# Performance work log

Hardware: AMD Instinct MI355X
Metric: run time of the kernel (lower is better)

Reference implementation:

```python
import jax, jax.numpy as jnp
import numpy as np

N = 50000
E = 1600000
# pna_deg histogram: all 50000 nodes have in-degree 32
_DEG_HIST = np.zeros(33, dtype=np.float64); _DEG_HIST[32] = N
AVG_DEG_LOG = float((np.log(np.arange(33) + 1.0) * _DEG_HIST).sum() / _DEG_HIST.sum())


def _segment_softmax(scores, seg, num_segments):
    # PyG softmax: subtract per-segment max, exp, normalize (+1e-16)
    m = jax.ops.segment_max(scores, seg, num_segments)
    e = jnp.exp(scores - m[seg])
    s = jax.ops.segment_sum(e, seg, num_segments)
    return e / (s[seg] + 1e-16)


def _gatv2(x, src, dst, edge_attr, Wl, bl, Wr, br, We, att, bias, H, C, n):
    xl = (x @ Wl + bl).reshape(n, H, C)   # source transform
    xr = (x @ Wr + br).reshape(n, H, C)   # target transform
    ee = (edge_attr @ We).reshape(-1, H, C)
    m = jax.nn.leaky_relu(xl[src] + xr[dst] + ee, negative_slope=0.2)  # [E,H,C]
    alpha = jnp.einsum('ehc,hc->eh', m, att)
    alpha = _segment_softmax(alpha, dst, n)
    out = jax.ops.segment_sum(xl[src] * alpha[:, :, None], dst, n)     # [n,H,C]
    return out.reshape(n, H * C) + bias


def setup_inputs() -> dict:
    key = jax.random.key(0)
    ks = jax.random.split(key, 20)
    x = jax.random.normal(ks[0], (N, 5), jnp.float32)
    src = jax.random.randint(ks[1], (E,), 0, N, jnp.int32)
    dst = ((src + 1 + jax.random.randint(ks[2], (E,), 0, N - 1, jnp.int32)) % N).astype(jnp.int32)
    edge_index = jnp.stack([src, dst])
    edge_weights = jax.random.uniform(ks[3], (E,), jnp.float32)

    def g(k, fi, fo):
        return (jax.random.normal(k, (fi, fo), jnp.float32) / np.sqrt(fi)).astype(jnp.float32)

    return dict(
        x=x, edge_index=edge_index, edge_weights=edge_weights,
        W_ee=g(ks[4], 1, 5), b_ee=jnp.zeros(5, jnp.float32),
        W_pre=g(ks[5], 15, 5), b_pre=jnp.zeros(5, jnp.float32),
        W_post=g(ks[6], 65, 8), b_post=jnp.zeros(8, jnp.float32),
        W_pna=g(ks[7], 8, 8), b_pna=jnp.zeros(8, jnp.float32),
        W1l=g(ks[8], 8, 16), b1l=jnp.zeros(16, jnp.float32),
        W1r=g(ks[9], 8, 16), b1r=jnp.zeros(16, jnp.float32),
        W1e=g(ks[10], 1, 16),
        att1=(jax.random.normal(ks[11], (4, 4), jnp.float32) * 0.5),
        bias1=jnp.zeros(16, jnp.float32),
        W2l=g(ks[12], 16, 32), b2l=jnp.zeros(32, jnp.float32),
        W2r=g(ks[13], 16, 32), b2r=jnp.zeros(32, jnp.float32),
        W2e=g(ks[14], 1, 32),
        att2=(jax.random.normal(ks[15], (4, 8), jnp.float32) / np.sqrt(8.0)).astype(jnp.float32),
        bias2=jnp.zeros(32, jnp.float32),
        Wn=g(ks[16], 32, 32), bn=jnp.zeros(32, jnp.float32),
        We_fc=g(ks[17], 65, 32), be_fc=jnp.zeros(32, jnp.float32),
    )


def reference(x, edge_index, edge_weights,
              W_ee, b_ee, W_pre, b_pre, W_post, b_post, W_pna, b_pna,
              W1l, b1l, W1r, b1r, W1e, att1, bias1,
              W2l, b2l, W2r, b2r, W2e, att2, bias2,
              Wn, bn, We_fc, be_fc):
    n = x.shape[0]
    src, dst = edge_index[0], edge_index[1]
    ea = edge_weights.reshape(-1, 1)  # [E,1]

    # ---------- PNAConv (towers=1, pre/post = single Linear) ----------
    enc = ea @ W_ee + b_ee                               # edge encoder [E,5]
    h = jnp.concatenate([x[dst], x[src], enc], axis=1)   # [x_i, x_j, e] -> [E,15]
    m = h @ W_pre + b_pre                                # [E,5]
    cnt = jax.ops.segment_sum(jnp.ones((m.shape[0],), m.dtype), dst, n)
    cntc = jnp.maximum(cnt, 1.0)[:, None]
    mean = jax.ops.segment_sum(m, dst, n) / cntc
    mean_sq = jax.ops.segment_sum(m * m, dst, n) / cntc
    std = jnp.sqrt(jax.nn.relu(mean_sq - mean * mean) + 1e-5)
    has = (cnt > 0)[:, None]
    mn = jnp.where(has, jax.ops.segment_min(m, dst, n), 0.0)
    mx = jnp.where(has, jax.ops.segment_max(m, dst, n), 0.0)
    agg = jnp.concatenate([mean, mn, mx, std], axis=1)   # [N,20]
    amp = jnp.log(jnp.maximum(cnt, 1.0) + 1.0)[:, None] / AVG_DEG_LOG
    out = jnp.concatenate([x, agg, agg * amp, agg / amp], axis=1)  # [N,65]
    nf = (out @ W_post + b_post) @ W_pna + b_pna         # [N,8]

    # ---------- self loops for GATv2 (fill_value='mean') ----------
    loop = jnp.arange(n, dtype=src.dtype)
    src_sl = jnp.concatenate([src, loop])
    dst_sl = jnp.concatenate([dst, loop])
    ea_mean = jax.ops.segment_sum(ea, dst, n) / cntc     # per-dst mean edge attr
    ea_sl = jnp.concatenate([ea, ea_mean], axis=0)

    nf = jax.nn.relu(_gatv2(nf, src_sl, dst_sl, ea_sl, W1l, b1l, W1r, b1r, W1e, att1, bias1, 4, 4, n))
    nf = jax.nn.relu(_gatv2(nf, src_sl, dst_sl, ea_sl, W2l, b2l, W2r, b2r, W2e, att2, bias2, 4, 8, n))
    nf = jax.nn.relu(nf @ Wn + bn)                       # [N,32]

    ef = jnp.concatenate([ea, nf[src], nf[dst]], axis=1) # [E,65]
    scores = ef @ We_fc + be_fc                          # [E,32]
    s0 = _segment_softmax(scores[:, 0], src, n)          # node_wise_softmax over src
    s1 = _segment_softmax(scores[:, 1], src, n)
    return scores.at[:, 0].set(s0).at[:, 1].set(s1)
```

## Files before the change

kernel.cpp:

```cpp
#include <hip/hip_runtime.h>
#include <math.h>

#define NN 50000
#define NE 1600000
#define AVG_DEG_LOG 3.4965075614664802f
#define NBIN 196
#define CHUNK 4096
#define NCHUNK 391

typedef float f4v __attribute__((ext_vector_type(4)));
typedef _Float16 h4v __attribute__((ext_vector_type(4)));

__device__ __forceinline__ float lrelu(float x){ return x > 0.f ? x : 0.2f*x; }
__device__ __forceinline__ float relu(float x){ return x > 0.f ? x : 0.f; }

__device__ __forceinline__ int ent_node(int2 ent){ return ent.x & 0xFFFF; }
__device__ __forceinline__ int ent_eid(int2 ent){
    return (int)(((unsigned)ent.x >> 16) | ((((unsigned)ent.y >> 19) & 31u) << 16));
}
__device__ __forceinline__ float ent_w(int2 ent){
    return ((float)((unsigned)ent.y & 0x7FFFFu) + 0.5f) * (1.0f/524288.0f);
}
__device__ __forceinline__ unsigned quant_w(float w){
    unsigned wq = (unsigned)(w * 524288.f);
    return wq > 524287u ? 524287u : wq;
}
__device__ __forceinline__ int cent_node(int e){ return e & 0xFFFF; }
__device__ __forceinline__ float cent_w(int e){
    return ((float)(((unsigned)e >> 16) & 0xFFFFu) + 0.5f) * (1.0f/65536.0f);
}
__device__ __forceinline__ unsigned fenc(float f){
    unsigned b = __float_as_uint(f);
    return (b & 0x80000000u) ? ~b : (b | 0x80000000u);
}
__device__ __forceinline__ float fdec(unsigned u){
    unsigned b = (u & 0x80000000u) ? (u & 0x7FFFFFFFu) : ~u;
    return __uint_as_float(b);
}


__global__ __launch_bounds__(256) void k_hist(const int* __restrict__ src, const int* __restrict__ dst,
                                              int* __restrict__ histD, int* __restrict__ histS){
    __shared__ int hd[NBIN], hs[NBIN];
    for (int t=threadIdx.x; t<NBIN; t+=256){ hd[t]=0; hs[t]=0; }
    __syncthreads();
// ... 4 lines not shown
        atomicAdd(&hs[src[e]>>8], 1);
    }
    __syncthreads();
    for (int t=threadIdx.x; t<NBIN; t+=256){
        histD[t*NCHUNK+chunk] = hd[t];
        histS[t*NCHUNK+chunk] = hs[t];
    }
}

__global__ __launch_bounds__(256) void k_binsum(const int* __restrict__ histD, const int* __restrict__ histS,
                                                int* __restrict__ binTotal){
    __shared__ int wsum[4];
    int dir = blockIdx.x / NBIN, bin = blockIdx.x % NBIN;
    const int* hist = dir ? histS : histD;
    int s = 0;
    for (int t=threadIdx.x; t<NCHUNK; t+=256) s += hist[bin*NCHUNK + t];
    #pragma unroll
    for (int st=32; st>=1; st>>=1) s += __shfl_xor(s, st);
    if ((threadIdx.x & 63) == 0) wsum[threadIdx.x>>6] = s;
    __syncthreads();
    if (threadIdx.x == 0) binTotal[dir*NBIN + bin] = wsum[0]+wsum[1]+wsum[2]+wsum[3];
}

__global__ __launch_bounds__(256) void k_scanbins(const int* __restrict__ binTotal,
                                                  int* __restrict__ binStartD, int* __restrict__ binStartS){
    __shared__ int wsums[4];
    int tid = threadIdx.x, lane = tid & 63, wv = tid >> 6;
    for (int dir = 0; dir < 2; ++dir){
        int* binStart = dir ? binStartS : binStartD;
        int v = (tid < NBIN) ? binTotal[dir*NBIN + tid] : 0;
        int sc = v;
        for (int d = 1; d < 64; d <<= 1){
            int t = __shfl_up(sc, d, 64);
            if (lane >= d) sc += t;
        }
        if (lane == 63) wsums[wv] = sc;
        __syncthreads();
        int woff = 0;
        #pragma unroll
        for (int k = 0; k < 4; ++k) woff += (k < wv) ? wsums[k] : 0;
        int excl = woff + sc - v;
        if (tid < NBIN) binStart[tid] = excl;
        if (tid == 0) binStart[NBIN] = NE;
        __syncthreads();
    }
}

__global__ __launch_bounds__(256) void k_chunkpfx(const int* __restrict__ histD, const int* __restrict__ histS,
                                                  const int* __restrict__ binStartD, const int* __restrict__ binStartS,
                                                  int* __restrict__ baseD, int* __restrict__ baseS){
    __shared__ int wsums[4];
    int dir = blockIdx.x / NBIN, bin = blockIdx.x % NBIN;
    const int* hist = dir ? histS : histD;
    const int* binStart = dir ? binStartS : binStartD;
    int* base = dir ? baseS : baseD;
    int tid = threadIdx.x, lane = tid & 63, wv = tid >> 6;
    int i0 = tid*2, i1 = tid*2+1;
    int a = (i0 < NCHUNK) ? hist[bin*NCHUNK + i0] : 0;
    int b = (i1 < NCHUNK) ? hist[bin*NCHUNK + i1] : 0;
    int v = a + b;
    int sc = v;
    for (int d = 1; d < 64; d <<= 1){
        int t = __shfl_up(sc, d, 64);
        if (lane >= d) sc += t;
    }
    if (lane == 63) wsums[wv] = sc;
    __syncthreads();
    int woff = 0;
    #pragma unroll
    for (int k = 0; k < 4; ++k) woff += (k < wv) ? wsums[k] : 0;
    int excl = binStart[bin] + woff + sc - v;
    if (i0 < NCHUNK) base[bin*NCHUNK + i0] = excl;
    if (i1 < NCHUNK) base[bin*NCHUNK + i1] = excl + a;
}

__global__ __launch_bounds__(256) void k_coarse(const int* __restrict__ src, const int* __restrict__ dst,
                                                const float* __restrict__ ea,
                                                const int* __restrict__ baseD, const int* __restrict__ baseS,
                                                int2* __restrict__ cD, int2* __restrict__ cS){
    __shared__ int curd[NBIN], curs[NBIN];
    int chunk = blockIdx.x;
    for (int t=threadIdx.x; t<NBIN; t+=256){
        curd[t] = baseD[t*NCHUNK+chunk];
        curs[t] = baseS[t*NCHUNK+chunk];
    }
    __syncthreads();
    int e0 = chunk*CHUNK, e1 = min(e0+CHUNK, NE);
    for (int e=e0+threadIdx.x; e<e1; e+=256){
        int s = src[e], d = dst[e];
        unsigned wq = quant_w(ea[e]);
        unsigned elo = (unsigned)(e & 0xFFFF) << 16;
        unsigned ehi = ((unsigned)e >> 16) << 19;
        int pd = atomicAdd(&curd[d>>8], 1);
        cD[pd] = make_int2((int)((unsigned)s | elo), (int)(((unsigned)(d & 255) << 24) | ehi | wq));
        int ps = atomicAdd(&curs[s>>8], 1);
        cS[ps] = make_int2((int)((unsigned)d | elo), (int)(((unsigned)(s & 255) << 24) | ehi | wq));
    }
}

__global__ __launch_bounds__(256) void k_fine_d(const int2* __restrict__ cin,
                                                const int* __restrict__ binStart,
                                                int2* __restrict__ bout,
                                                int* __restrict__ cnt, int* __restrict__ off){
    __shared__ int h[256], cur[256];
    __shared__ int ws4[4];
    int bin = blockIdx.x;
    int S = binStart[bin], E = binStart[bin+1];
    h[threadIdx.x] = 0;
    __syncthreads();
    for (int i = S + threadIdx.x; i < E; i += 256){
        unsigned y = (unsigned)cin[i].y;
        atomicAdd(&h[y >> 24], 1);
    }
    __syncthreads();
    int v = h[threadIdx.x];
    int lane = threadIdx.x & 63, wv = threadIdx.x >> 6;
    int sc = v;
    for (int d = 1; d < 64; d <<= 1){
        int t = __shfl_up(sc, d, 64);
        if (lane >= d) sc += t;
    }
    if (lane == 63) ws4[wv] = sc;
    __syncthreads();
    int woff = 0;
    #pragma unroll
    for (int k = 0; k < 4; ++k) woff += (k < wv) ? ws4[k] : 0;
    int excl = woff + sc - v;
    cur[threadIdx.x] = S + excl;
    int node = (bin << 8) + threadIdx.x;
    if (node < NN){ cnt[node] = v; off[node] = S + excl; }
    __syncthreads();
    for (int i = S + threadIdx.x; i < E; i += 256){
        int2 ent = cin[i];
        unsigned y = (unsigned)ent.y;
        int local = y >> 24;
        int pos = atomicAdd(&cur[local], 1);
        bout[pos] = make_int2(ent.x, (int)(y & 0x00FFFFFFu));
    }
}


__global__ void k_zero(int* cnt_d, int* cnt_s){
    int i = blockIdx.x*blockDim.x + threadIdx.x;
    if (i < NN){ cnt_d[i]=0; cnt_s[i]=0; }
}

__global__ void k_count(const int* __restrict__ src, const int* __restrict__ dst,
                        int* cnt_d, int* cnt_s){
    int e = blockIdx.x*blockDim.x + threadIdx.x;
    if (e >= NE) return;
    atomicAdd(&cnt_d[dst[e]], 1);
    atomicAdd(&cnt_s[src[e]], 1);
}

__global__ __launch_bounds__(1024) void k_scanCSR(const int* __restrict__ cnt_d, const int* __restrict__ cnt_s,
                                                  int* off_d, int* cur_d, int* off_s, int* cur_s){
    __shared__ int wsums[16];
    __shared__ int carry_s;
    const int tid = threadIdx.x, lane = tid & 63, wv = tid >> 6;
    const int pass = blockIdx.x;
// ... 15 lines not shown
            if (lane >= d) sc += t;
        }
        if (lane == 63) wsums[wv] = sc;
        __syncthreads();
        int woff = 0;
        #pragma unroll
        for (int k = 0; k < 16; ++k) woff += (k < wv) ? wsums[k] : 0;
        int carry_in = carry_s;
        __syncthreads();
        if (tid == 1023) carry_s = carry_in + woff + sc;
        int excl = carry_in + woff + (sc - tsum);
        int e0 = excl, e1 = e0+v0, e2 = e1+v1, e3 = e2+v2;
        if (i0+0 < NN){ off[i0+0]=e0; cur[i0+0]=e0; }
        if (i0+1 < NN){ off[i0+1]=e1; cur[i0+1]=e1; }
        if (i0+2 < NN){ off[i0+2]=e2; cur[i0+2]=e2; }
        if (i0+3 < NN){ off[i0+3]=e3; cur[i0+3]=e3; }
        __syncthreads();
    }
}

__global__ void k_scatter(const int* __restrict__ src, const int* __restrict__ dst,
                          const float* __restrict__ ea,
                          int* cur_d, int* cur_s,
                          int2* bktd, int* bkts){
    int e = blockIdx.x*blockDim.x + threadIdx.x;
    if (e >= NE) return;
    int s = src[e], d = dst[e];
    unsigned wq = quant_w(ea[e]);
    unsigned elo = (unsigned)(e & 0xFFFF) << 16;
    unsigned yv  = (((unsigned)e >> 16) << 19) | wq;
    int p = atomicAdd(&cur_d[d], 1);
    bktd[p] = make_int2((int)((unsigned)s | elo), (int)yv);
    int q = atomicAdd(&cur_s[s], 1);
    bkts[q] = (int)(((unsigned)d & 0xFFFFu) | ((wq >> 3) << 16));
}

__global__ __launch_bounds__(256) void k_pna(
    const float* __restrict__ x,
    const int* __restrict__ cnt_d, const int* __restrict__ off_d,
    const int2* __restrict__ bktd,
    const float* __restrict__ W_ee, const float* __restrict__ b_ee,
    const float* __restrict__ W_pre, const float* __restrict__ b_pre,
    const float* __restrict__ W_post, const float* __restrict__ b_post,
    const float* __restrict__ W_pna, const float* __restrict__ b_pna,
    const float* __restrict__ W1l, const float* __restrict__ b1l,
    const float* __restrict__ W1r, const float* __restrict__ b1r,
    float* __restrict__ xl1, float* __restrict__ xr1, float* __restrict__ ea_mean)
{
    __shared__ float sWpre[75], sWpost[520], sWpna[64], sW1l[128], sW1r[128];
    __shared__ float sbpre[5], sWee[5], sbee[5], sbpost[8], sbpna[8], sb1l[16], sb1r[16];
    for (int t=threadIdx.x; t<75;  t+=256) sWpre[t]=W_pre[t];
    for (int t=threadIdx.x; t<520; t+=256) sWpost[t]=W_post[t];
    for (int t=threadIdx.x; t<64;  t+=256) sWpna[t]=W_pna[t];
    for (int t=threadIdx.x; t<128; t+=256){ sW1l[t]=W1l[t]; sW1r[t]=W1r[t]; }
    if (threadIdx.x<5){ sbpre[threadIdx.x]=b_pre[threadIdx.x]; sWee[threadIdx.x]=W_ee[threadIdx.x]; sbee[threadIdx.x]=b_ee[threadIdx.x]; }
    if (threadIdx.x<8){ sbpost[threadIdx.x]=b_post[threadIdx.x]; sbpna[threadIdx.x]=b_pna[threadIdx.x]; }
    if (threadIdx.x<16){ sb1l[threadIdx.x]=b1l[threadIdx.x]; sb1r[threadIdx.x]=b1r[threadIdx.x]; }
    __syncthreads();
    int node = blockIdx.x*32 + (threadIdx.x>>3);
    if (node >= NN) return;
    int g = threadIdx.x & 7;
    float xd[5];
    #pragma unroll
    for (int k=0;k<5;k++) xd[k] = x[node*5+k];
    float cb[5], c1v[5];
    #pragma unroll
    for (int c=0;c<5;c++){
        float a = sbpre[c], b = 0.f;
        #pragma unroll
        for (int k=0;k<5;k++){
            a += xd[k]*sWpre[k*5+c];
            a += sbee[k]*sWpre[(10+k)*5+c];
            b += sWee[k]*sWpre[(10+k)*5+c];
        }
        cb[c]=a; c1v[c]=b;
    }
    int deg = cnt_d[node], base = off_d[node];
    float sum[5], ssq[5], mn[5], mx[5];
    #pragma unroll
    for (int c=0;c<5;c++){ sum[c]=0.f; ssq[c]=0.f; mn[c]=1e30f; mx[c]=-1e30f; }
    float wsum = 0.f;
    for (int j=g; j<deg; j+=8){
        int2 ent = bktd[base+j];
        int s = ent_node(ent);
        float w = ent_w(ent);
        wsum += w;
        float xs[5];
        #pragma unroll
        for (int k=0;k<5;k++) xs[k] = x[s*5+k];
        #pragma unroll
        for (int c=0;c<5;c++){
            float m = cb[c] + w*c1v[c];
            #pragma unroll
            for (int k=0;k<5;k++) m += xs[k]*sWpre[(5+k)*5+c];
            sum[c]+=m; ssq[c]+=m*m; mn[c]=fminf(mn[c],m); mx[c]=fmaxf(mx[c],m);
        }
    }
    #pragma unroll
    for (int st=1; st<8; st<<=1){
        #pragma unroll
        for (int c=0;c<5;c++){
            sum[c] += __shfl_xor(sum[c], st);
            ssq[c] += __shfl_xor(ssq[c], st);
            mn[c] = fminf(mn[c], __shfl_xor(mn[c], st));
            mx[c] = fmaxf(mx[c], __shfl_xor(mx[c], st));
        }
        wsum += __shfl_xor(wsum, st);
    }
// ... 15 lines not shown
    for (int j=0;j<20;j++){ feat[25+j]=feat[5+j]*amp; feat[45+j]=feat[5+j]/amp; }
    float t = sbpost[g];
    #pragma unroll
    for (int k=0;k<65;k++) t += feat[k]*sWpost[k*8+g];
    float nf = sbpna[g];
    #pragma unroll
    for (int k=0;k<8;k++) nf += __shfl(t, k, 8) * sWpna[k*8+g];
    float nfk[8];
    #pragma unroll
    for (int k=0;k<8;k++) nfk[k] = __shfl(nf, k, 8);
    #pragma unroll
    for (int u=0;u<2;u++){
        int o = 2*g+u;
        float a=sb1l[o], b2=sb1r[o];
        #pragma unroll
        for (int k=0;k<8;k++){ a += nfk[k]*sW1l[k*16+o]; b2 += nfk[k]*sW1r[k*16+o]; }
        xl1[node*16+o]=a; xr1[node*16+o]=b2;
    }
    if (g==0) ea_mean[node] = wsum/cc;
}

__global__ __launch_bounds__(256) void k_gat1(
    const int* __restrict__ cnt_d, const int* __restrict__ off_d,
    const int2* __restrict__ bktd,
    const float* __restrict__ xl1, const float* __restrict__ xr1,
    const float* __restrict__ ea_mean,
    const float* __restrict__ We1, const float* __restrict__ att1, const float* __restrict__ bias1,
    const float* __restrict__ W2l, const float* __restrict__ b2l,
    const float* __restrict__ W2r, const float* __restrict__ b2r,
    _Float16* __restrict__ xl2h, float* __restrict__ xr2)
{
    __shared__ float sWe[16], sAtt[16], sBias[16], sW2l[512], sW2r[512], sb2l[32], sb2r[32];
    for (int t=threadIdx.x; t<512; t+=256){ sW2l[t]=W2l[t]; sW2r[t]=W2r[t]; }
    if (threadIdx.x<16){ sWe[threadIdx.x]=We1[threadIdx.x]; sAtt[threadIdx.x]=att1[threadIdx.x]; sBias[threadIdx.x]=bias1[threadIdx.x]; }
    if (threadIdx.x<32){ sb2l[threadIdx.x]=b2l[threadIdx.x]; sb2r[threadIdx.x]=b2r[threadIdx.x]; }
    __syncthreads();
    int node = blockIdx.x*32 + (threadIdx.x>>3);
    if (node >= NN) return;
    int g = threadIdx.x & 7;
    float xr[16];
    #pragma unroll
    for (int k=0;k<4;k++){
        float4 v = *(const float4*)(xr1 + node*16 + k*4);
        xr[k*4]=v.x; xr[k*4+1]=v.y; xr[k*4+2]=v.z; xr[k*4+3]=v.w;
    }
    int deg = cnt_d[node], base = off_d[node];
    float eam = ea_mean[node];
    float m[4], ss[4], acc[16];
    #pragma unroll
    for (int h=0;h<4;h++){ m[h]=-1e30f; ss[h]=0.f; }
    #pragma unroll
    for (int k=0;k<16;k++) acc[k]=0.f;
    for (int j=g; j<=deg; j+=8){
        bool selfe = (j==deg);
        int s; float w;
        if (selfe){ s = node; w = eam; }
        else { int2 ent = bktd[base+j]; s = ent_node(ent); w = ent_w(ent); }
        float xls[16];
        #pragma unroll
        for (int k=0;k<4;k++){
            float4 v = *(const float4*)(xl1 + s*16 + k*4);
            xls[k*4]=v.x; xls[k*4+1]=v.y; xls[k*4+2]=v.z; xls[k*4+3]=v.w;
        }
        #pragma unroll
        for (int h=0;h<4;h++){
            float a = 0.f;
            #pragma unroll
            for (int ch=0;ch<4;ch++){
                int idx = h*4+ch;
                a += lrelu(xls[idx] + xr[idx] + w*sWe[idx]) * sAtt[idx];
            }
            float mn2 = fmaxf(m[h], a);
            float corr = __expf(m[h]-mn2);
            float p = __expf(a-mn2);
            ss[h] = ss[h]*corr + p;
            #pragma unroll
            for (int ch=0;ch<4;ch++){
                int idx = h*4+ch;
                acc[idx] = acc[idx]*corr + p*xls[idx];
            }
// ... 21 lines not shown
    float nf1[16];
    #pragma unroll
    for (int h=0;h<4;h++){
        float den = ss[h] + 1e-16f;
        #pragma unroll
        for (int ch=0;ch<4;ch++){
            int idx=h*4+ch;
            nf1[idx] = relu(acc[idx]/den + sBias[idx]);
        }
    }
    #pragma unroll
    for (int u=0;u<4;u++){
        int o = g + 8*u;
        float a=sb2l[o], b=sb2r[o];
        #pragma unroll
        for (int k=0;k<16;k++){ a += nf1[k]*sW2l[k*32+o]; b += nf1[k]*sW2r[k*32+o]; }
        xl2h[(size_t)node*32+o] = (_Float16)a;
        xr2[node*32+o]=b;
    }
}

__global__ __launch_bounds__(256) void k_gat2(
    const int* __restrict__ cnt_d, const int* __restrict__ off_d,
    const int2* __restrict__ bktd,
    const _Float16* __restrict__ xl2h, const float* __restrict__ xr2,
    const float* __restrict__ ea_mean,
    const float* __restrict__ We2, const float* __restrict__ att2, const float* __restrict__ bias2,
    const float* __restrict__ Wn, const float* __restrict__ bn,
    const float* __restrict__ We_fc,
    _Float16* __restrict__ Ps16, float* __restrict__ Pd,
    float* __restrict__ Ps01, float* __restrict__ Pd01)
{
    __shared__ float sWe[32], sAtt[32], sBias[32], sWn[1024], sbn[32];
    __shared__ float sWsrc[1024], sWdst[1024];
    for (int t=threadIdx.x; t<1024; t+=256){
        sWn[t]=Wn[t];
        sWsrc[t]=We_fc[32 + t];
        sWdst[t]=We_fc[33*32 + t];
    }
    if (threadIdx.x<32){ sWe[threadIdx.x]=We2[threadIdx.x]; sAtt[threadIdx.x]=att2[threadIdx.x];
                         sBias[threadIdx.x]=bias2[threadIdx.x]; sbn[threadIdx.x]=bn[threadIdx.x]; }
    __syncthreads();
    int node = blockIdx.x*32 + (threadIdx.x>>3);
    if (node >= NN) return;
    int g = threadIdx.x & 7;
    float xr[32];
    #pragma unroll
    for (int k=0;k<8;k++){
        float4 v = *(const float4*)(xr2 + node*32 + k*4);
        xr[k*4]=v.x; xr[k*4+1]=v.y; xr[k*4+2]=v.z; xr[k*4+3]=v.w;
    }
    int deg = cnt_d[node], base = off_d[node];
    float eam = ea_mean[node];
    float m[4], ss[4], acc[32];
    #pragma unroll
    for (int h=0;h<4;h++){ m[h]=-1e30f; ss[h]=0.f; }
    #pragma unroll
    for (int k=0;k<32;k++) acc[k]=0.f;
    for (int j=g; j<=deg; j+=8){
        bool selfe = (j==deg);
        int s; float w;
        if (selfe){ s = node; w = eam; }
        else { int2 ent = bktd[base+j]; s = ent_node(ent); w = ent_w(ent); }
        float xls[32];
        const h4v* xp = (const h4v*)(xl2h + (size_t)s*32);
        #pragma unroll
        for (int k=0;k<8;k++){
            h4v hv = xp[k];
            xls[k*4]   = (float)hv.x;
            xls[k*4+1] = (float)hv.y;
            xls[k*4+2] = (float)hv.z;
            xls[k*4+3] = (float)hv.w;
        }
        #pragma unroll
        for (int h=0;h<4;h++){
            float a = 0.f;
            #pragma unroll
            for (int ch=0;ch<8;ch++){
                int idx = h*8+ch;
                a += lrelu(xls[idx] + xr[idx] + w*sWe[idx]) * sAtt[idx];
            }
            float mn2 = fmaxf(m[h], a);
            float corr = __expf(m[h]-mn2);
            float p = __expf(a-mn2);
            ss[h] = ss[h]*corr + p;
            #pragma unroll
            for (int ch=0;ch<8;ch++){
                int idx = h*8+ch;
                acc[idx] = acc[idx]*corr + p*xls[idx];
            }
            m[h] = mn2;
        }
    }
    #pragma unroll
    for (int st=1; st<8; st<<=1){
// ... 24 lines not shown
        }
    }
    float mine[4];
    #pragma unroll
    for (int u=0;u<4;u++){
        int oo = g + 8*u;
        float a = sbn[oo];
        #pragma unroll
        for (int k=0;k<32;k++) a += nf2[k]*sWn[k*32+oo];
        mine[u] = relu(a);
    }
    float nfn[32];
    #pragma unroll
    for (int k=0;k<32;k++) nfn[k] = __shfl(mine[k>>3], k&7, 8);
    float pa[4], pb[4];
    #pragma unroll
    for (int u=0;u<4;u++){
        int oo = g + 8*u;
        float a=0.f, b=0.f;
        #pragma unroll
        for (int k=0;k<32;k++){ a += nfn[k]*sWsrc[k*32+oo]; b += nfn[k]*sWdst[k*32+oo]; }
        pa[u]=a; pb[u]=b;
        Ps16[(size_t)node*32+oo] = (_Float16)a;
        Pd[node*32+oo]=b;
    }
    float ps0=__shfl(pa[0],0,8), ps1=__shfl(pa[0],1,8);
    float pd0=__shfl(pb[0],0,8), pd1=__shfl(pb[0],1,8);
    if (g==0){
        *(float2*)(Ps01 + node*2) = make_float2(ps0, ps1);
        *(float2*)(Pd01 + node*2) = make_float2(pd0, pd1);
    }
}

__global__ __launch_bounds__(1024) void k_src_bins(
    const int2* __restrict__ cS, const int* __restrict__ binStartS,
    const float* __restrict__ Ps01, const float* __restrict__ Pd01,
    const float* __restrict__ We_fc, const float* __restrict__ be_fc,
    float* __restrict__ smax, float* __restrict__ sden)
{
    __shared__ float sPs0[256], sPs1[256];
    __shared__ unsigned sM0[256], sM1[256];
    __shared__ float sS0[256], sS1[256];
    __shared__ float cW00, cW01, cbe0, cbe1;
    int bin = blockIdx.x, tid = threadIdx.x;
    if (tid == 0){ cW00=We_fc[0]; cW01=We_fc[1]; cbe0=be_fc[0]; cbe1=be_fc[1]; }
    if (tid < 256){
        int node = (bin<<8) + tid;
        float2 p = (node < NN) ? *(const float2*)(Ps01 + node*2) : make_float2(0.f,0.f);
        sPs0[tid]=p.x; sPs1[tid]=p.y;
        sM0[tid]=fenc(-1e30f); sM1[tid]=fenc(-1e30f);
        sS0[tid]=0.f; sS1[tid]=0.f;
    }
    __syncthreads();
    int S = binStartS[bin], E = binStartS[bin+1];
    for (int i = S + tid; i < E; i += 1024){
        int2 ent = cS[i];
        unsigned y = (unsigned)ent.y;
        int local = y >> 24;
        int d = ent.x & 0xFFFF;
        float w = ((float)(y & 0x7FFFFu) + 0.5f) * (1.0f/524288.0f);
        float2 q = *(const float2*)(Pd01 + d*2);
        float a0 = cbe0 + sPs0[local] + w*cW00 + q.x;
        float a1 = cbe1 + sPs1[local] + w*cW01 + q.y;
        atomicMax(&sM0[local], fenc(a0));
        atomicMax(&sM1[local], fenc(a1));
    }
    __syncthreads();
    for (int i = S + tid; i < E; i += 1024){
        int2 ent = cS[i];
        unsigned y = (unsigned)ent.y;
        int local = y >> 24;
        int d = ent.x & 0xFFFF;
        float w = ((float)(y & 0x7FFFFu) + 0.5f) * (1.0f/524288.0f);
        float2 q = *(const float2*)(Pd01 + d*2);
        float a0 = cbe0 + sPs0[local] + w*cW00 + q.x;
        float a1 = cbe1 + sPs1[local] + w*cW01 + q.y;
        atomicAdd(&sS0[local], __expf(a0 - fdec(sM0[local])));
        atomicAdd(&sS1[local], __expf(a1 - fdec(sM1[local])));
    }
    __syncthreads();
    if (tid < 256){
        int node = (bin<<8) + tid;
        if (node < NN){
            smax[node*2]   = fdec(sM0[tid]);
            smax[node*2+1] = fdec(sM1[tid]);
            sden[node*2]   = sS0[tid];
            sden[node*2+1] = sS1[tid];
        }
    }
}

__global__ __launch_bounds__(256) void k_src(
    const int* __restrict__ cnt_s, const int* __restrict__ off_s,
    const int* __restrict__ bkts,
    const float* __restrict__ Ps01, const float* __restrict__ Pd01,
    const float* __restrict__ We_fc, const float* __restrict__ be_fc,
    float* __restrict__ smax, float* __restrict__ sden)
{
    __shared__ float sW00, sW01, sbe0, sbe1;
    if (threadIdx.x == 0){ sW00=We_fc[0]; sW01=We_fc[1]; sbe0=be_fc[0]; sbe1=be_fc[1]; }
    __syncthreads();
    int node = blockIdx.x*32 + (threadIdx.x>>3);
    if (node >= NN) return;
    int g = threadIdx.x & 7;
    float2 p = *(const float2*)(Ps01 + node*2);
    float base0 = sbe0 + p.x, base1 = sbe1 + p.y;
    int deg = cnt_s[node], base = off_s[node];
    float m0=-1e30f, m1=-1e30f, s0=0.f, s1=0.f;
    for (int j=g; j<deg; j+=8){
        int ent = bkts[base+j];
        int d = cent_node(ent);
        float w = cent_w(ent);
        float2 q = *(const float2*)(Pd01 + d*2);
        float a0 = base0 + w*sW00 + q.x;
        float a1 = base1 + w*sW01 + q.y;
        float mn0 = fmaxf(m0, a0);
        s0 = s0*__expf(m0-mn0) + __expf(a0-mn0); m0 = mn0;
        float mn1 = fmaxf(m1, a1);
        s1 = s1*__expf(m1-mn1) + __expf(a1-mn1); m1 = mn1;
    }
    #pragma unroll
    for (int st=1; st<8; st<<=1){
        float mo = __shfl_xor(m0, st), so = __shfl_xor(s0, st);
        float mn = fmaxf(m0, mo);
        s0 = s0*__expf(m0-mn) + so*__expf(mo-mn); m0 = mn;
        mo = __shfl_xor(m1, st); so = __shfl_xor(s1, st);
        mn = fmaxf(m1, mo);
        s1 = s1*__expf(m1-mn) + so*__expf(mo-mn); m1 = mn;
    }
    if (g==0){ smax[node*2]=m0; smax[node*2+1]=m1; sden[node*2]=s0; sden[node*2+1]=s1; }
}

__global__ __launch_bounds__(256) void k_scC2(
    const int* __restrict__ cnt_d, const int* __restrict__ off_d,
    const int2* __restrict__ bktd,
    const _Float16* __restrict__ Ps16, const float* __restrict__ Pd,
    const float* __restrict__ We_fc, const float* __restrict__ be_fc,
    const float* __restrict__ smax, const float* __restrict__ sden,
    float* __restrict__ out)
{
    __shared__ float sW0[32], sB[32];
    if (threadIdx.x < 32){ sW0[threadIdx.x]=We_fc[threadIdx.x]; sB[threadIdx.x]=be_fc[threadIdx.x]; }
    __syncthreads();
    int node = blockIdx.x*32 + (threadIdx.x>>3);
    if (node >= NN) return;
    int g = threadIdx.x & 7;
    float4 pd = *(const float4*)(Pd + (size_t)node*32 + g*4);
    float4 w0 = *(const float4*)(sW0 + g*4);
    float4 b0 = *(const float4*)(sB + g*4);
    b0.x += pd.x; b0.y += pd.y; b0.z += pd.z; b0.w += pd.w;
    int deg = cnt_d[node], base = off_d[node];
    for (int j=0; j<deg; ++j){
        int2 ent = bktd[base+j];
        int s = ent_node(ent);
        int e = ent_eid(ent);
        float w = ent_w(ent);
        h4v hv = *(const h4v*)(Ps16 + (size_t)s*32 + g*4);
        float ox = b0.x + w*w0.x + (float)hv.x;
        float oy = b0.y + w*w0.y + (float)hv.y;
        float oz = b0.z + w*w0.z + (float)hv.z;
        float ow = b0.w + w*w0.w + (float)hv.w;
        if (g == 0){
            float2 sm = *(const float2*)(smax + s*2);
            float2 sd = *(const float2*)(sden + s*2);
            ox = __expf(ox - sm.x) / (sd.x + 1e-16f);
            oy = __expf(oy - sm.y) / (sd.y + 1e-16f);
        }
        f4v ov; ov.x = ox; ov.y = oy; ov.z = oz; ov.w = ow;
        __builtin_nontemporal_store(ov, (f4v*)(out + (size_t)e*32 + g*4));
    }
}

extern "C" void kernel_launch(void* const* d_in, const int* in_sizes, int n_in,
                              void* d_out, int out_size, void* d_ws, size_t ws_size,
                              hipStream_t stream) {
    const float* x     = (const float*)d_in[0];
    const int*   ei    = (const int*)  d_in[1];
    const float* ea    = (const float*)d_in[2];
    const float* W_ee  = (const float*)d_in[3];  const float* b_ee  = (const float*)d_in[4];
    const float* W_pre = (const float*)d_in[5];  const float* b_pre = (const float*)d_in[6];
    const float* W_post= (const float*)d_in[7];  const float* b_post= (const float*)d_in[8];
    const float* W_pna = (const float*)d_in[9];  const float* b_pna = (const float*)d_in[10];
    const float* W1l   = (const float*)d_in[11]; const float* b1l   = (const float*)d_in[12];
    const float* W1r   = (const float*)d_in[13]; const float* b1r   = (const float*)d_in[14];
    const float* W1e   = (const float*)d_in[15]; const float* att1  = (const float*)d_in[16];
    const float* bias1 = (const float*)d_in[17];
    const float* W2l   = (const float*)d_in[18]; const float* b2l   = (const float*)d_in[19];
    const float* W2r   = (const float*)d_in[20]; const float* b2r   = (const float*)d_in[21];
    const float* W2e   = (const float*)d_in[22]; const float* att2  = (const float*)d_in[23];
    const float* bias2 = (const float*)d_in[24];
    const float* Wn    = (const float*)d_in[25]; const float* bn    = (const float*)d_in[26];
    const float* We_fc = (const float*)d_in[27]; const float* be_fc = (const float*)d_in[28];
    const int* src = ei;
    const int* dst = ei + NE;
    float* out = (float*)d_out;

    float* ws = (float*)d_ws;
    size_t o = 0;
    auto A = [&](size_t n){ size_t r = o; o = (o + n + 63) & ~(size_t)63; return r; };
    int*   cnt_d  = (int*)(ws + A(NN));
    int*   off_d  = (int*)(ws + A(NN));
    int*   cnt_s  = (int*)(ws + A(NN));
    int*   off_s  = (int*)(ws + A(NN));
    int*   cur_d  = (int*)(ws + A(NN));
    int*   cur_s  = (int*)(ws + A(NN));
    float* xl1    =        ws + A((size_t)NN*16);
    float* xr1    =        ws + A((size_t)NN*16);
    _Float16* xl2h = (_Float16*)(ws + A((size_t)NN*16));
    float* xr2    =        ws + A((size_t)NN*32);
    _Float16* Ps16 = (_Float16*)(ws + A((size_t)NN*16));
    float* Pd     =        ws + A((size_t)NN*32);
    float* ea_mean=        ws + A(NN);
    float* Ps01   =        ws + A((size_t)NN*2);
    float* Pd01   =        ws + A((size_t)NN*2);
    float* smax   =        ws + A((size_t)NN*2);
    float* sden   =        ws + A((size_t)NN*2);
    int*   histD  = (int*)(ws + A((size_t)NBIN*NCHUNK));
    int*   histS  = (int*)(ws + A((size_t)NBIN*NCHUNK));
    int*   baseD  = (int*)(ws + A((size_t)NBIN*NCHUNK));
    int*   baseS  = (int*)(ws + A((size_t)NBIN*NCHUNK));
    int*   binTotal  = (int*)(ws + A(2*NBIN));
    int*   binStartD = (int*)(ws + A(NBIN+1));
    int*   binStartS = (int*)(ws + A(NBIN+1));
    int2*  bufX = (int2*)(ws + A(2*(size_t)NE));
    int*   bktsC = (int*)(ws + A((size_t)NE));
    size_t o_fallback = o;
    int2*  bufY = (int2*)(ws + A(2*(size_t)NE));
    int2*  bufZ = (int2*)(ws + A(2*(size_t)NE));
    size_t o_sort = o;
    bool sortmode = (ws_size >= o_sort * sizeof(float));
    if (!sortmode && ws_size < o_fallback * sizeof(float)) return;

    const int BS = 256;
    const int gridE = (NE + BS - 1)/BS;
    const int gridN = (NN + BS - 1)/BS;
    const int gridO = (NN + 31)/32;

    int2* bktd = bufX;
    if (sortmode){
        k_hist<<<NCHUNK, BS, 0, stream>>>(src, dst, histD, histS);
        k_binsum<<<2*NBIN, BS, 0, stream>>>(histD, histS, binTotal);
        k_scanbins<<<1, BS, 0, stream>>>(binTotal, binStartD, binStartS);
        k_chunkpfx<<<2*NBIN, BS, 0, stream>>>(histD, histS, binStartD, binStartS, baseD, baseS);
        k_coarse<<<NCHUNK, BS, 0, stream>>>(src, dst, ea, baseD, baseS, bufY, bufZ);
        k_fine_d<<<NBIN, BS, 0, stream>>>(bufY, binStartD, bufX, cnt_d, off_d);
    } else {
        k_zero<<<gridN, BS, 0, stream>>>(cnt_d, cnt_s);
        k_count<<<gridE, BS, 0, stream>>>(src, dst, cnt_d, cnt_s);
        k_scanCSR<<<2, 1024, 0, stream>>>(cnt_d, cnt_s, off_d, cur_d, off_s, cur_s);
        k_scatter<<<gridE, BS, 0, stream>>>(src, dst, ea, cur_d, cur_s, bufX, bktsC);
    }
    k_pna<<<gridO, BS, 0, stream>>>(x, cnt_d, off_d, bktd,
                                    W_ee, b_ee, W_pre, b_pre, W_post, b_post, W_pna, b_pna,
                                    W1l, b1l, W1r, b1r, xl1, xr1, ea_mean);
    k_gat1<<<gridO, BS, 0, stream>>>(cnt_d, off_d, bktd, xl1, xr1, ea_mean,
                                     W1e, att1, bias1, W2l, b2l, W2r, b2r, xl2h, xr2);
    k_gat2<<<gridO, BS, 0, stream>>>(cnt_d, off_d, bktd, xl2h, xr2, ea_mean,
                                     W2e, att2, bias2, Wn, bn, We_fc,
                                     Ps16, Pd, Ps01, Pd01);
    if (sortmode){
        k_src_bins<<<NBIN, 1024, 0, stream>>>(bufZ, binStartS, Ps01, Pd01, We_fc, be_fc, smax, sden);
    } else {
        k_src<<<gridO, BS, 0, stream>>>(cnt_s, off_s, bktsC, Ps01, Pd01, We_fc, be_fc, smax, sden);
    }
    k_scC2<<<gridO, BS, 0, stream>>>(cnt_d, off_d, bktd, Ps16, Pd, We_fc, be_fc, smax, sden, out);
}
```

Measured before the change: 298.8 us.

## Compact adjacency, fuse bin scan, and compute edge scores in original edge order

The final edge-score kernel now runs one thread per edge in original order, reading src/dst/ea directly instead of walking the dst-sorted adjacency, so output writes become coalesced and edge ids no longer need to be packed. This lets the dst adjacency shrink from int2 to a single int with 16-bit quantized weight, and Pd is stored as fp16. The separate bin scan kernel is folded into the chunk-prefix kernel, softmax stats are packed into one float4, and k_src_bins caches the first few computed scores in registers to avoid recomputing them. The cost is lower-precision Pd and edge weight in the fine path, and gathers of Ps16/Pd16 by random src/dst.

```diff
diff --git a/kernel.cpp b/kernel.cpp
--- a/kernel.cpp
+++ b/kernel.cpp
@@ -9,18 +9,11 @@
 #define NCHUNK 391
 
 typedef float f4v __attribute__((ext_vector_type(4)));
-typedef _Float16 h4v __attribute__((ext_vector_type(4)));
+typedef _Float16 h8v __attribute__((ext_vector_type(8)));
 
 __device__ __forceinline__ float lrelu(float x){ return x > 0.f ? x : 0.2f*x; }
 __device__ __forceinline__ float relu(float x){ return x > 0.f ? x : 0.f; }
 
-__device__ __forceinline__ int ent_node(int2 ent){ return ent.x & 0xFFFF; }
-__device__ __forceinline__ int ent_eid(int2 ent){
-    return (int)(((unsigned)ent.x >> 16) | ((((unsigned)ent.y >> 19) & 31u) << 16));
-}
-__device__ __forceinline__ float ent_w(int2 ent){
-    return ((float)((unsigned)ent.y & 0x7FFFFu) + 0.5f) * (1.0f/524288.0f);
-}
 __device__ __forceinline__ unsigned quant_w(float w){
     unsigned wq = (unsigned)(w * 524288.f);
     return wq > 524287u ? 524287u : wq;
@@ -71,39 +64,33 @@
     if (threadIdx.x == 0) binTotal[dir*NBIN + bin] = wsum[0]+wsum[1]+wsum[2]+wsum[3];
 }
 
-__global__ __launch_bounds__(256) void k_scanbins(const int* __restrict__ binTotal,
-                                                  int* __restrict__ binStartD, int* __restrict__ binStartS){
-    __shared__ int wsums[4];
-    int tid = threadIdx.x, lane = tid & 63, wv = tid >> 6;
-    for (int dir = 0; dir < 2; ++dir){
-        int* binStart = dir ? binStartS : binStartD;
-        int v = (tid < NBIN) ? binTotal[dir*NBIN + tid] : 0;
-        int sc = v;
-        for (int d = 1; d < 64; d <<= 1){
-            int t = __shfl_up(sc, d, 64);
-            if (lane >= d) sc += t;
-        }
-        if (lane == 63) wsums[wv] = sc;
-        __syncthreads();
-        int woff = 0;
-        #pragma unroll
-        for (int k = 0; k < 4; ++k) woff += (k < wv) ? wsums[k] : 0;
-        int excl = woff + sc - v;
-        if (tid < NBIN) binStart[tid] = excl;
-        if (tid == 0) binStart[NBIN] = NE;
-        __syncthreads();
-    }
-}
-
 __global__ __launch_bounds__(256) void k_chunkpfx(const int* __restrict__ histD, const int* __restrict__ histS,
-                                                  const int* __restrict__ binStartD, const int* __restrict__ binStartS,
+                                                  const int* __restrict__ binTotal,
+                                                  int* __restrict__ binStartD, int* __restrict__ binStartS,
                                                   int* __restrict__ baseD, int* __restrict__ baseS){
     __shared__ int wsums[4];
+    __shared__ int sbase;
     int dir = blockIdx.x / NBIN, bin = blockIdx.x % NBIN;
     const int* hist = dir ? histS : histD;
-    const int* binStart = dir ? binStartS : binStartD;
+    int* binStart = dir ? binStartS : binStartD;
     int* base = dir ? baseS : baseD;
     int tid = threadIdx.x, lane = tid & 63, wv = tid >> 6;
+    {
+        int s = 0;
+        for (int k = tid; k < bin; k += 256) s += binTotal[dir*NBIN + k];
+        #pragma unroll
+        for (int st=32; st>=1; st>>=1) s += __shfl_xor(s, st);
+        if (lane == 0) wsums[wv] = s;
+        __syncthreads();
+        if (tid == 0){
+            sbase = wsums[0]+wsums[1]+wsums[2]+wsums[3];
+            binStart[bin] = sbase;
+            if (bin == 0) binStart[NBIN] = NE;
+        }
+        __syncthreads();
+    }
+    int bS = sbase;
+    __syncthreads();
     int i0 = tid*2, i1 = tid*2+1;
     int a = (i0 < NCHUNK) ? hist[bin*NCHUNK + i0] : 0;
     int b = (i1 < NCHUNK) ? hist[bin*NCHUNK + i1] : 0;
@@ -118,7 +105,7 @@
     int woff = 0;
     #pragma unroll
     for (int k = 0; k < 4; ++k) woff += (k < wv) ? wsums[k] : 0;
-    int excl = binStart[bin] + woff + sc - v;
+    int excl = bS + woff + sc - v;
     if (i0 < NCHUNK) base[bin*NCHUNK + i0] = excl;
     if (i1 < NCHUNK) base[bin*NCHUNK + i1] = excl + a;
 }
@@ -138,19 +125,17 @@
     for (int e=e0+threadIdx.x; e<e1; e+=256){
         int s = src[e], d = dst[e];
         unsigned wq = quant_w(ea[e]);
-        unsigned elo = (unsigned)(e & 0xFFFF) << 16;
-        unsigned ehi = ((unsigned)e >> 16) << 19;
         int pd = atomicAdd(&curd[d>>8], 1);
-        cD[pd] = make_int2((int)((unsigned)s | elo), (int)(((unsigned)(d & 255) << 24) | ehi | wq));
+        cD[pd] = make_int2(s, (int)(((unsigned)(d & 255) << 24) | wq));
         int ps = atomicAdd(&curs[s>>8], 1);
-        cS[ps] = make_int2((int)((unsigned)d | elo), (int)(((unsigned)(s & 255) << 24) | ehi | wq));
-    }
-}
-
-__global__ __launch_bounds__(256) void k_fine_d(const int2* __restrict__ cin,
-                                                const int* __restrict__ binStart,
-                                                int2* __restrict__ bout,
-                                                int* __restrict__ cnt, int* __restrict__ off){
+        cS[ps] = make_int2(d, (int)(((unsigned)(s & 255) << 24) | wq));
+    }
+}
+
+__global__ __launch_bounds__(256) void k_fine(const int2* __restrict__ cin,
+                                              const int* __restrict__ binStart,
+                                              int* __restrict__ bout,
+                                              int* __restrict__ cnt, int* __restrict__ off){
     __shared__ int h[256], cur[256];
     __shared__ int ws4[4];
     int bin = blockIdx.x;
@@ -184,7 +169,8 @@
         unsigned y = (unsigned)ent.y;
         int local = y >> 24;
         int pos = atomicAdd(&cur[local], 1);
-        bout[pos] = make_int2(ent.x, (int)(y & 0x00FFFFFFu));
+        unsigned wq16 = (y & 0x7FFFFu) >> 3;
+        bout[pos] = (int)(((unsigned)ent.x & 0xFFFFu) | (wq16 << 16));
     }
 }
 
@@ -246,23 +232,21 @@
 __global__ void k_scatter(const int* __restrict__ src, const int* __restrict__ dst,
                           const float* __restrict__ ea,
                           int* cur_d, int* cur_s,
-                          int2* bktd, int* bkts){
+                          int* bktd, int* bkts){
     int e = blockIdx.x*blockDim.x + threadIdx.x;
     if (e >= NE) return;
     int s = src[e], d = dst[e];
-    unsigned wq = quant_w(ea[e]);
-    unsigned elo = (unsigned)(e & 0xFFFF) << 16;
-    unsigned yv  = (((unsigned)e >> 16) << 19) | wq;
+    unsigned wq16 = quant_w(ea[e]) >> 3;
     int p = atomicAdd(&cur_d[d], 1);
-    bktd[p] = make_int2((int)((unsigned)s | elo), (int)yv);
+    bktd[p] = (int)(((unsigned)s & 0xFFFFu) | (wq16 << 16));
     int q = atomicAdd(&cur_s[s], 1);
-    bkts[q] = (int)(((unsigned)d & 0xFFFFu) | ((wq >> 3) << 16));
+    bkts[q] = (int)(((unsigned)d & 0xFFFFu) | (wq16 << 16));
 }
 
 __global__ __launch_bounds__(256) void k_pna(
     const float* __restrict__ x,
     const int* __restrict__ cnt_d, const int* __restrict__ off_d,
-    const int2* __restrict__ bktd,
+    const int* __restrict__ adjC,
     const float* __restrict__ W_ee, const float* __restrict__ b_ee,
     const float* __restrict__ W_pre, const float* __restrict__ b_pre,
     const float* __restrict__ W_post, const float* __restrict__ b_post,
@@ -305,9 +289,9 @@
     for (int c=0;c<5;c++){ sum[c]=0.f; ssq[c]=0.f; mn[c]=1e30f; mx[c]=-1e30f; }
     float wsum = 0.f;
     for (int j=g; j<deg; j+=8){
-        int2 ent = bktd[base+j];
-        int s = ent_node(ent);
-        float w = ent_w(ent);
+        int ent = adjC[base+j];
+        int s = cent_node(ent);
+        float w = cent_w(ent);
         wsum += w;
         float xs[5];
         #pragma unroll
@@ -369,7 +353,7 @@
 
 __global__ __launch_bounds__(256) void k_gat1(
     const int* __restrict__ cnt_d, const int* __restrict__ off_d,
-    const int2* __restrict__ bktd,
+    const int* __restrict__ adjC,
     const float* __restrict__ xl1, const float* __restrict__ xr1,
     const float* __restrict__ ea_mean,
     const float* __restrict__ We1, const float* __restrict__ att1, const float* __restrict__ bias1,
@@ -402,7 +386,7 @@
         bool selfe = (j==deg);
         int s; float w;
         if (selfe){ s = node; w = eam; }
-        else { int2 ent = bktd[base+j]; s = ent_node(ent); w = ent_w(ent); }
+        else { int ent = adjC[base+j]; s = cent_node(ent); w = cent_w(ent); }
         float xls[16];
         #pragma unroll
         for (int k=0;k<4;k++){
@@ -470,13 +454,13 @@
 
 __global__ __launch_bounds__(256) void k_gat2(
     const int* __restrict__ cnt_d, const int* __restrict__ off_d,
-    const int2* __restrict__ bktd,
+    const int* __restrict__ adjC,
     const _Float16* __restrict__ xl2h, const float* __restrict__ xr2,
     const float* __restrict__ ea_mean,
     const float* __restrict__ We2, const float* __restrict__ att2, const float* __restrict__ bias2,
     const float* __restrict__ Wn, const float* __restrict__ bn,
     const float* __restrict__ We_fc,
-    _Float16* __restrict__ Ps16, float* __restrict__ Pd,
+    _Float16* __restrict__ Ps16, _Float16* __restrict__ Pd16,
     float* __restrict__ Ps01, float* __restrict__ Pd01)
 {
     __shared__ float sWe[32], sAtt[32], sBias[32], sWn[1024], sbn[32];
@@ -509,16 +493,14 @@
         bool selfe = (j==deg);
         int s; float w;
         if (selfe){ s = node; w = eam; }
-        else { int2 ent = bktd[base+j]; s = ent_node(ent); w = ent_w(ent); }
+        else { int ent = adjC[base+j]; s = cent_node(ent); w = cent_w(ent); }
         float xls[32];
-        const h4v* xp = (const h4v*)(xl2h + (size_t)s*32);
-        #pragma unroll
-        for (int k=0;k<8;k++){
-            h4v hv = xp[k];
-            xls[k*4]   = (float)hv.x;
-            xls[k*4+1] = (float)hv.y;
-            xls[k*4+2] = (float)hv.z;
-            xls[k*4+3] = (float)hv.w;
+        const h8v* xp = (const h8v*)(xl2h + (size_t)s*32);
+        #pragma unroll
+        for (int k=0;k<4;k++){
+            h8v hv = xp[k];
+            #pragma unroll
+            for (int u=0;u<8;u++) xls[k*8+u] = (float)hv[u];
         }
         #pragma unroll
         for (int h=0;h<4;h++){
@@ -589,7 +571,7 @@
         for (int k=0;k<32;k++){ a += nfn[k]*sWsrc[k*32+oo]; b += nfn[k]*sWdst[k*32+oo]; }
         pa[u]=a; pb[u]=b;
         Ps16[(size_t)node*32+oo] = (_Float16)a;
-        Pd[node*32+oo]=b;
+        Pd16[(size_t)node*32+oo] = (_Float16)b;
     }
     float ps0=__shfl(pa[0],0,8), ps1=__shfl(pa[0],1,8);
     float pd0=__shfl(pb[0],0,8), pd1=__shfl(pb[0],1,8);
@@ -603,7 +585,7 @@
     const int2* __restrict__ cS, const int* __restrict__ binStartS,
     const float* __restrict__ Ps01, const float* __restrict__ Pd01,
     const float* __restrict__ We_fc, const float* __restrict__ be_fc,
-    float* __restrict__ smax, float* __restrict__ sden)
+    float4* __restrict__ ssd)
 {
     __shared__ float sPs0[256], sPs1[256];
     __shared__ unsigned sM0[256], sM1[256];
@@ -620,40 +602,61 @@
     }
     __syncthreads();
     int S = binStartS[bin], E = binStartS[bin+1];
-    for (int i = S + tid; i < E; i += 1024){
+    const int REG = 9;
+    float ra0[REG], ra1[REG]; int rl[REG];
+    int n = 0;
+    {
+        int idx = S + tid;
+        #pragma unroll
+        for (int it = 0; it < REG; ++it){
+            if (idx < E){
+                int2 ent = cS[idx];
+                unsigned y = (unsigned)ent.y;
+                int local = y >> 24;
+                int d = ent.x;
+                float w = ((float)(y & 0x7FFFFu) + 0.5f) * (1.0f/524288.0f);
+                float2 q = *(const float2*)(Pd01 + d*2);
+                float a0 = cbe0 + sPs0[local] + w*cW00 + q.x;
+                float a1 = cbe1 + sPs1[local] + w*cW01 + q.y;
+                ra0[it]=a0; ra1[it]=a1; rl[it]=local; n = it+1;
+                atomicMax(&sM0[local], fenc(a0));
+                atomicMax(&sM1[local], fenc(a1));
+            }
+            idx += 1024;
+        }
+        for (int i = S + tid + REG*1024; i < E; i += 1024){
+            int2 ent = cS[i];
+            unsigned y = (unsigned)ent.y;
+            int local = y >> 24;
+            int d = ent.x;
+            float w = ((float)(y & 0x7FFFFu) + 0.5f) * (1.0f/524288.0f);
+            float2 q = *(const float2*)(Pd01 + d*2);
+            atomicMax(&sM0[local], fenc(cbe0 + sPs0[local] + w*cW00 + q.x));
+            atomicMax(&sM1[local], fenc(cbe1 + sPs1[local] + w*cW01 + q.y));
+        }
+    }
+    __syncthreads();
+    #pragma unroll
+    for (int it = 0; it < REG; ++it){
+        if (it < n){
+            atomicAdd(&sS0[rl[it]], __expf(ra0[it] - fdec(sM0[rl[it]])));
+            atomicAdd(&sS1[rl[it]], __expf(ra1[it] - fdec(sM1[rl[it]])));
+        }
+    }
+    for (int i = S + tid + REG*1024; i < E; i += 1024){
         int2 ent = cS[i];
         unsigned y = (unsigned)ent.y;
         int local = y >> 24;
-        int d = ent.x & 0xFFFF;
+        int d = ent.x;
         float w = ((float)(y & 0x7FFFFu) + 0.5f) * (1.0f/524288.0f);
         float2 q = *(const float2*)(Pd01 + d*2);
-        float a0 = cbe0 + sPs0[local] + w*cW00 + q.x;
-        float a1 = cbe1 + sPs1[local] + w*cW01 + q.y;
-        atomicMax(&sM0[local], fenc(a0));
-        atomicMax(&sM1[local], fenc(a1));
-    }
-    __syncthreads();
-    for (int i = S + tid; i < E; i += 1024){
-        int2 ent = cS[i];
-        unsigned y = (unsigned)ent.y;
-        int local = y >> 24;
-        int d = ent.x & 0xFFFF;
-        float w = ((float)(y & 0x7FFFFu) + 0.5f) * (1.0f/524288.0f);
-        float2 q = *(const float2*)(Pd01 + d*2);
-        float a0 = cbe0 + sPs0[local] + w*cW00 + q.x;
-        float a1 = cbe1 + sPs1[local] + w*cW01 + q.y;
-        atomicAdd(&sS0[local], __expf(a0 - fdec(sM0[local])));
-        atomicAdd(&sS1[local], __expf(a1 - fdec(sM1[local])));
+        atomicAdd(&sS0[local], __expf(cbe0 + sPs0[local] + w*cW00 + q.x - fdec(sM0[local])));
+        atomicAdd(&sS1[local], __expf(cbe1 + sPs1[local] + w*cW01 + q.y - fdec(sM1[local])));
     }
     __syncthreads();
     if (tid < 256){
         int node = (bin<<8) + tid;
-        if (node < NN){
-            smax[node*2]   = fdec(sM0[tid]);
-            smax[node*2+1] = fdec(sM1[tid]);
-            sden[node*2]   = sS0[tid];
-            sden[node*2+1] = sS1[tid];
-        }
+        if (node < NN) ssd[node] = make_float4(fdec(sM0[tid]), fdec(sM1[tid]), sS0[tid], sS1[tid]);
     }
 }
 
@@ -662,7 +665,7 @@
     const int* __restrict__ bkts,
     const float* __restrict__ Ps01, const float* __restrict__ Pd01,
     const float* __restrict__ We_fc, const float* __restrict__ be_fc,
-    float* __restrict__ smax, float* __restrict__ sden)
+    float4* __restrict__ ssd)
 {
     __shared__ float sW00, sW01, sbe0, sbe1;
     if (threadIdx.x == 0){ sW00=We_fc[0]; sW01=We_fc[1]; sbe0=be_fc[0]; sbe1=be_fc[1]; }
@@ -695,46 +698,43 @@
         mn = fmaxf(m1, mo);
         s1 = s1*__expf(m1-mn) + so*__expf(mo-mn); m1 = mn;
     }
-    if (g==0){ smax[node*2]=m0; smax[node*2+1]=m1; sden[node*2]=s0; sden[node*2+1]=s1; }
-}
-
-__global__ __launch_bounds__(256) void k_scC2(
-    const int* __restrict__ cnt_d, const int* __restrict__ off_d,
-    const int2* __restrict__ bktd,
-    const _Float16* __restrict__ Ps16, const float* __restrict__ Pd,
+    if (g==0) ssd[node] = make_float4(m0, m1, s0, s1);
+}
+
+__global__ __launch_bounds__(256) void k_scF(
+    const int* __restrict__ src, const int* __restrict__ dst, const float* __restrict__ ea,
+    const _Float16* __restrict__ Ps16, const _Float16* __restrict__ Pd16,
     const float* __restrict__ We_fc, const float* __restrict__ be_fc,
-    const float* __restrict__ smax, const float* __restrict__ sden,
+    const float4* __restrict__ ssd,
     float* __restrict__ out)
 {
     __shared__ float sW0[32], sB[32];
     if (threadIdx.x < 32){ sW0[threadIdx.x]=We_fc[threadIdx.x]; sB[threadIdx.x]=be_fc[threadIdx.x]; }
     __syncthreads();
-    int node = blockIdx.x*32 + (threadIdx.x>>3);
-    if (node >= NN) return;
-    int g = threadIdx.x & 7;
-    float4 pd = *(const float4*)(Pd + (size_t)node*32 + g*4);
-    float4 w0 = *(const float4*)(sW0 + g*4);
-    float4 b0 = *(const float4*)(sB + g*4);
-    b0.x += pd.x; b0.y += pd.y; b0.z += pd.z; b0.w += pd.w;
-    int deg = cnt_d[node], base = off_d[node];
-    for (int j=0; j<deg; ++j){
-        int2 ent = bktd[base+j];
-        int s = ent_node(ent);
-        int e = ent_eid(ent);
-        float w = ent_w(ent);
-        h4v hv = *(const h4v*)(Ps16 + (size_t)s*32 + g*4);
-        float ox = b0.x + w*w0.x + (float)hv.x;
-        float oy = b0.y + w*w0.y + (float)hv.y;
-        float oz = b0.z + w*w0.z + (float)hv.z;
-        float ow = b0.w + w*w0.w + (float)hv.w;
-        if (g == 0){
-            float2 sm = *(const float2*)(smax + s*2);
-            float2 sd = *(const float2*)(sden + s*2);
-            ox = __expf(ox - sm.x) / (sd.x + 1e-16f);
-            oy = __expf(oy - sm.y) / (sd.y + 1e-16f);
-        }
-        f4v ov; ov.x = ox; ov.y = oy; ov.z = oz; ov.w = ow;
-        __builtin_nontemporal_store(ov, (f4v*)(out + (size_t)e*32 + g*4));
+    int e = blockIdx.x*blockDim.x + threadIdx.x;
+    if (e >= NE) return;
+    int s = src[e], d = dst[e];
+    float w = ea[e];
+    const h8v* ps = (const h8v*)(Ps16 + (size_t)s*32);
+    const h8v* pd = (const h8v*)(Pd16 + (size_t)d*32);
+    float o[32];
+    #pragma unroll
+    for (int k=0;k<4;k++){
+        h8v a = ps[k], b = pd[k];
+        #pragma unroll
+        for (int u=0;u<8;u++){
+            int j = k*8+u;
+            o[j] = sB[j] + w*sW0[j] + (float)a[u] + (float)b[u];
+        }
+    }
+    float4 v = ssd[s];
+    o[0] = __expf(o[0] - v.x) / (v.z + 1e-16f);
+    o[1] = __expf(o[1] - v.y) / (v.w + 1e-16f);
+    float* op = out + (size_t)e*32;
+    #pragma unroll
+    for (int j=0;j<8;j++){
+        f4v ov; ov.x=o[j*4]; ov.y=o[j*4+1]; ov.z=o[j*4+2]; ov.w=o[j*4+3];
+        __builtin_nontemporal_store(ov, (f4v*)(op + j*4));
     }
 }
 
@@ -776,12 +776,11 @@
     _Float16* xl2h = (_Float16*)(ws + A((size_t)NN*16));
     float* xr2    =        ws + A((size_t)NN*32);
     _Float16* Ps16 = (_Float16*)(ws + A((size_t)NN*16));
-    float* Pd     =        ws + A((size_t)NN*32);
+    _Float16* Pd16 = (_Float16*)(ws + A((size_t)NN*16));
     float* ea_mean=        ws + A(NN);
     float* Ps01   =        ws + A((size_t)NN*2);
     float* Pd01   =        ws + A((size_t)NN*2);
-    float* smax   =        ws + A((size_t)NN*2);
-    float* sden   =        ws + A((size_t)NN*2);
+    float4* ssd   = (float4*)(ws + A((size_t)NN*4));
     int*   histD  = (int*)(ws + A((size_t)NBIN*NCHUNK));
     int*   histS  = (int*)(ws + A((size_t)NBIN*NCHUNK));
     int*   baseD  = (int*)(ws + A((size_t)NBIN*NCHUNK));
@@ -789,7 +788,7 @@
     int*   binTotal  = (int*)(ws + A(2*NBIN));
     int*   binStartD = (int*)(ws + A(NBIN+1));
     int*   binStartS = (int*)(ws + A(NBIN+1));
-    int2*  bufX = (int2*)(ws + A(2*(size_t)NE));
+    int*   adjC  = (int*)(ws + A((size_t)NE));
     int*   bktsC = (int*)(ws + A((size_t)NE));
     size_t o_fallback = o;
     int2*  bufY = (int2*)(ws + A(2*(size_t)NE));
@@ -803,32 +802,30 @@
     const int gridN = (NN + BS - 1)/BS;
     const int gridO = (NN + 31)/32;
 
-    int2* bktd = bufX;
     if (sortmode){
         k_hist<<<NCHUNK, BS, 0, stream>>>(src, dst, histD, histS);
         k_binsum<<<2*NBIN, BS, 0, stream>>>(histD, histS, binTotal);
-        k_scanbins<<<1, BS, 0, stream>>>(binTotal, binStartD, binStartS);
-        k_chunkpfx<<<2*NBIN, BS, 0, stream>>>(histD, histS, binStartD, binStartS, baseD, baseS);
+        k_chunkpfx<<<2*NBIN, BS, 0, stream>>>(histD, histS, binTotal, binStartD, binStartS, baseD, baseS);
         k_coarse<<<NCHUNK, BS, 0, stream>>>(src, dst, ea, baseD, baseS, bufY, bufZ);
-        k_fine_d<<<NBIN, BS, 0, stream>>>(bufY, binStartD, bufX, cnt_d, off_d);
+        k_fine<<<NBIN, BS, 0, stream>>>(bufY, binStartD, adjC, cnt_d, off_d);
     } else {
         k_zero<<<gridN, BS, 0, stream>>>(cnt_d, cnt_s);
         k_count<<<gridE, BS, 0, stream>>>(src, dst, cnt_d, cnt_s);
         k_scanCSR<<<2, 1024, 0, stream>>>(cnt_d, cnt_s, off_d, cur_d, off_s, cur_s);
-        k_scatter<<<gridE, BS, 0, stream>>>(src, dst, ea, cur_d, cur_s, bufX, bktsC);
-    }
-    k_pna<<<gridO, BS, 0, stream>>>(x, cnt_d, off_d, bktd,
+        k_scatter<<<gridE, BS, 0, stream>>>(src, dst, ea, cur_d, cur_s, adjC, bktsC);
+    }
+    k_pna<<<gridO, BS, 0, stream>>>(x, cnt_d, off_d, adjC,
                                     W_ee, b_ee, W_pre, b_pre, W_post, b_post, W_pna, b_pna,
                                     W1l, b1l, W1r, b1r, xl1, xr1, ea_mean);
-    k_gat1<<<gridO, BS, 0, stream>>>(cnt_d, off_d, bktd, xl1, xr1, ea_mean,
+    k_gat1<<<gridO, BS, 0, stream>>>(cnt_d, off_d, adjC, xl1, xr1, ea_mean,
                                      W1e, att1, bias1, W2l, b2l, W2r, b2r, xl2h, xr2);
-    k_gat2<<<gridO, BS, 0, stream>>>(cnt_d, off_d, bktd, xl2h, xr2, ea_mean,
+    k_gat2<<<gridO, BS, 0, stream>>>(cnt_d, off_d, adjC, xl2h, xr2, ea_mean,
                                      W2e, att2, bias2, Wn, bn, We_fc,
-                                     Ps16, Pd, Ps01, Pd01);
+                                     Ps16, Pd16, Ps01, Pd01);
     if (sortmode){
-        k_src_bins<<<NBIN, 1024, 0, stream>>>(bufZ, binStartS, Ps01, Pd01, We_fc, be_fc, smax, sden);
+        k_src_bins<<<NBIN, 1024, 0, stream>>>(bufZ, binStartS, Ps01, Pd01, We_fc, be_fc, ssd);
     } else {
-        k_src<<<gridO, BS, 0, stream>>>(cnt_s, off_s, bktsC, Ps01, Pd01, We_fc, be_fc, smax, sden);
-    }
-    k_scC2<<<gridO, BS, 0, stream>>>(cnt_d, off_d, bktd, Ps16, Pd, We_fc, be_fc, smax, sden, out);
-}
+        k_src<<<gridO, BS, 0, stream>>>(cnt_s, off_s, bktsC, Ps01, Pd01, We_fc, be_fc, ssd);
+    }
+    k_scF<<<gridE, BS, 0, stream>>>(src, dst, ea, Ps16, Pd16, We_fc, be_fc, ssd, out);
+}
```

Measured after the change: 656.4 us. 2.2x slower.
